# Performance work log

Hardware: AMD Instinct MI355X
Metric: run time of the kernel (lower is better)

Reference implementation:

```python
import jax, jax.numpy as jnp
import numpy as np

B, L, E, H, D, DFF = 2, 2048, 1024, 16, 64, 4096
SCALE = D ** 0.5


def rmsnorm(x):
    # NOTE: original uses mean(x*x)**0.5 with no eps and no learned scale
    rms = jnp.sqrt(jnp.mean(x * x, axis=-1, keepdims=True))
    return x / rms


def alibi_matrix():
    i = jnp.arange(L)
    dists = -jnp.abs(i[None, :] - i[:, None]).astype(jnp.float32)  # [L, L]
    slopes = 2.0 ** (-jnp.linspace(1.0, 8.0, H))                   # [H]
    alibi = slopes[:, None, None] * dists                          # [H, L, L]
    causal = jnp.tril(jnp.ones((L, L), dtype=bool))
    return jnp.where(causal[None], alibi, -jnp.inf)[None]          # [1, H, L, L]


def setup_inputs() -> dict:
    key = jax.random.key(0)
    ks = jax.random.split(key, 16)
    s = 0.02
    return {
        "X": jax.random.normal(ks[0], (B, L, E), jnp.float32),
        "encoder_out": jax.random.normal(ks[1], (B, L, E), jnp.float32),
        # self-attention params
        "Wqkv": jax.random.normal(ks[2], (E, 3 * H * D), jnp.float32) * s,
        "bqkv": jnp.zeros((3 * H * D,), jnp.float32),
        "Wo_sa": jax.random.normal(ks[3], (H * D, E), jnp.float32) * s,
        "bo_sa": jnp.zeros((E,), jnp.float32),
        # cross-attention params (computed by torch module but its forward returns X, so unused)
        "Wq": jax.random.normal(ks[4], (E, H * D), jnp.float32) * s,
        "bq": jnp.zeros((H * D,), jnp.float32),
        "Wkv": jax.random.normal(ks[5], (E, 2 * H * D), jnp.float32) * s,
        "bkv": jnp.zeros((2 * H * D,), jnp.float32),
        "Wo_ca": jax.random.normal(ks[6], (H * D, E), jnp.float32) * s,
        "bo_ca": jnp.zeros((E,), jnp.float32),
        # GLU FFN params (bias=False)
        "Ww": jax.random.normal(ks[7], (E, DFF), jnp.float32) * s,
        "Wv": jax.random.normal(ks[8], (E, DFF), jnp.float32) * s,
        "Wout": jax.random.normal(ks[9], (DFF, E), jnp.float32) * s,
    }


def reference(X, encoder_out, Wqkv, bqkv, Wo_sa, bo_sa, Wq, bq, Wkv, bkv,
              Wo_ca, bo_ca, Ww, Wv, Wout):
    alibi = alibi_matrix()

    # ---- self-attention (pre-norm + residual) ----
    h = rmsnorm(X)
    qkv = (h @ Wqkv + bqkv).reshape(B, L, H, 3, D)
    Q, K, V = qkv[..., 0, :], qkv[..., 1, :], qkv[..., 2, :]      # [B, L, H, D]
    scores = jnp.einsum('blhd,bmhd->bhlm', Q, K) / SCALE + alibi  # [B, H, L, L]
    attn = jax.nn.softmax(scores, axis=-1)
    ctx = jnp.einsum('bhlm,bmhd->blhd', attn, V).reshape(B, L, H * D)
    X = X + ctx @ Wo_sa + bo_sa

    # ---- cross-attention stage ----
    # Faithful to source: CrossAttention.forward returns its input X (the
    # normalized tensor) rather than the attention output, so this block is
    # X + rmsnorm(X). Cross-attn params never affect the output.
    X = X + rmsnorm(X)

    # ---- GLU FFN (pre-norm + residual), exact (erf) GELU as in torch F.gelu ----
    h = rmsnorm(X)
    ff = jax.nn.gelu(h @ Ww, approximate=False) * (h @ Wv)
    X = X + ff @ Wout
    return X
```

## Files before the change

kernel.cpp:

```cpp
#include <hip/hip_runtime.h>

#define B_SZ 2
#define L_SEQ 2048
#define E_DIM 1024
#define NH 16
#define DH 64
#define DFF_DIM 4096
#define ROWS (B_SZ * L_SEQ)
#define NCID 80

typedef __attribute__((ext_vector_type(8))) short short8;
typedef __attribute__((ext_vector_type(4))) float f32x4;

__device__ __forceinline__ short f2bf(float f) {
  unsigned u = __builtin_bit_cast(unsigned, f);
  u = (u + 0x7FFFu + ((u >> 16) & 1u)) >> 16;
  return (short)u;
}
__device__ __forceinline__ float bf2f(short s) {
  unsigned u = ((unsigned)(unsigned short)s) << 16;
  return __builtin_bit_cast(float, u);
}

__device__ __forceinline__ float fast_gelu(float x) {
  float ax = fabsf(x) * 0.70710678118654752f;
  float t = __builtin_amdgcn_rcpf(__builtin_fmaf(0.3275911f, ax, 1.0f));
  float p = t * __builtin_fmaf(
                    t,
                    __builtin_fmaf(
                        t,
                        __builtin_fmaf(t,
                                       __builtin_fmaf(t, 1.061405429f,
                                                      -1.453152027f),
                                       1.421413741f),
                        -0.284496736f),
                    0.254829592f);
  float erf = 1.0f - p * __expf(-ax * ax);
  erf = copysignf(erf, x);
  return 0.5f * x * (1.0f + erf);
}

__device__ __forceinline__ void async_copy16(const void* g, void* l) {
  __builtin_amdgcn_global_load_lds(
      (const __attribute__((address_space(1))) void*)g,
      (__attribute__((address_space(3))) void*)l, 16, 0, 0);
}

__device__ __forceinline__ float block_sum256(float v) {
  __shared__ float sbuf[4];
#pragma unroll
  for (int off = 32; off > 0; off >>= 1) v += __shfl_xor(v, off, 64);
  int lane = threadIdx.x & 63, w = threadIdx.x >> 6;
  if (lane == 0) sbuf[w] = v;
  __syncthreads();
  return sbuf[0] + sbuf[1] + sbuf[2] + sbuf[3];
}

__global__ __launch_bounds__(256) void prep_all(
    const float* __restrict__ Wqkv, const float* __restrict__ Wo,
    const float* __restrict__ Ww, const float* __restrict__ Wv,
    const float* __restrict__ Wout, const float* __restrict__ X,
    short* __restrict__ Bqkv3, short* __restrict__ WoT,
    short* __restrict__ Bcat, short* __restrict__ WoutT,
    short* __restrict__ H) {
  __shared__ float tile[32][33];
  int b = blockIdx.x;
  if (b < 16384) {
    const float* W;
    short* Wt;
    int K, N, mode, bx, by;
    if (b < 3072) {
      W = Wqkv; Wt = Bqkv3; K = 1024; N = 3072; mode = 1;
      bx = b % 96; by = b / 96;
    } else if (b < 4096) {
      int c = b - 3072;
      W = Wo; Wt = WoT; K = 1024; N = 1024; mode = 1;
      bx = c & 31; by = c >> 5;
    } else if (b < 8192) {
      int c = b - 4096;
      W = Ww; Wt = Bcat; K = 1024; N = 4096; mode = 2;
      bx = c & 127; by = c >> 7;
    } else if (b < 12288) {
      int c = b - 8192;
      W = Wv; Wt = Bcat; K = 1024; N = 4096; mode = 3;
      bx = c & 127; by = c >> 7;
    } else {
      int c = b - 12288;
      W = Wout; Wt = WoutT; K = 4096; N = 1024; mode = 1;
      bx = c & 31; by = c >> 5;
    }
    int n0 = bx * 32, k0 = by * 32;
    int tx = threadIdx.x & 31, ty = threadIdx.x >> 5;
#pragma unroll
    for (int i = 0; i < 4; i++)
      tile[ty + 8 * i][tx] = W[(size_t)(k0 + ty + 8 * i) * N + n0 + tx];
    __syncthreads();
#pragma unroll
    for (int i = 0; i < 4; i++) {
      int n = n0 + ty + 8 * i;
      int orow = (mode == 1)
                     ? n
                     : ((n >> 5) * 64 + (n & 31) + (mode == 3 ? 32 : 0));
      Wt[(size_t)orow * K + k0 + tx] = f2bf(tile[tx][ty + 8 * i]);
    }
  } else {
    size_t row = b - 16384;
    float4 v = ((const float4*)(X + row * E_DIM))[threadIdx.x];
    float ss = v.x * v.x + v.y * v.y + v.z * v.z + v.w * v.w;
    ss = block_sum256(ss);
    float inv = rsqrtf(ss * (1.0f / E_DIM));
    short* h = H + row * E_DIM + (size_t)threadIdx.x * 4;
    h[0] = f2bf(v.x * inv);
    h[1] = f2bf(v.y * inv);
    h[2] = f2bf(v.z * inv);
    h[3] = f2bf(v.w * inv);
  }
}

__global__ __launch_bounds__(256) void resid_rms_fused(
    const float* __restrict__ X, const float* __restrict__ P0,
    const float* __restrict__ P1, const float* __restrict__ bias,
    float* __restrict__ Xout, short* __restrict__ H) {
  size_t row = blockIdx.x;
  int t = threadIdx.x;
  float4 v = ((const float4*)(X + row * E_DIM))[t];
  float4 a = ((const float4*)(P0 + row * E_DIM))[t];
  float4 b = ((const float4*)(P1 + row * E_DIM))[t];
  float4 c = ((const float4*)bias)[t];
  v.x += a.x + b.x + c.x;
  v.y += a.y + b.y + c.y;
  v.z += a.z + b.z + c.z;
  v.w += a.w + b.w + c.w;
  float ss = v.x * v.x + v.y * v.y + v.z * v.z + v.w * v.w;
  ss = block_sum256(ss);
  float inv = rsqrtf(ss * (1.0f / E_DIM));
  float4 o;
  o.x = v.x * (1.0f + inv);
  o.y = v.y * (1.0f + inv);
  o.z = v.z * (1.0f + inv);
  o.w = v.w * (1.0f + inv);
  ((float4*)(Xout + row * E_DIM))[t] = o;
  short* h = H + row * E_DIM + (size_t)t * 4;
  h[0] = f2bf(v.x * inv);
  h[1] = f2bf(v.y * inv);
  h[2] = f2bf(v.z * inv);
  h[3] = f2bf(v.w * inv);
}

__global__ __launch_bounds__(256) void add2_k(const float* __restrict__ P0,
                                              const float* __restrict__ P1,
                                              float* __restrict__ out) {
  size_t i = (size_t)blockIdx.x * 256 + threadIdx.x;
  float4 v = ((const float4*)out)[i];
  float4 a = ((const float4*)P0)[i];
  float4 b = ((const float4*)P1)[i];
  v.x += a.x + b.x;
  v.y += a.y + b.y;
  v.z += a.z + b.z;
  v.w += a.w + b.w;
  ((float4*)out)[i] = v;
}

__global__ __launch_bounds__(256, 2) void gemm_bt(
    const short* __restrict__ A, const short* __restrict__ Bt,
    const float* __restrict__ bias, void* __restrict__ out,
    void* __restrict__ out2, void* __restrict__ out3, int M, int N, int K,
    int epi, int ksplit) {
  __shared__ short smem[128 * 32 * 4];
  short* As0 = smem;
  short* Bs0 = smem + 4096;
  short* As1 = smem + 8192;
  short* Bs1 = smem + 12288;
  int t = threadIdx.x;
  int lane = t & 63;
  int quad = lane >> 4, l16 = lane & 15;
  int wave = t >> 6;
  int wr = wave >> 1, wc = wave & 1;
  int m0 = blockIdx.y * 128, n0 = blockIdx.x * 128;
  int klen = K / ksplit;
  int kstart = blockIdx.z * klen;

  f32x4 acc[4][4];
#pragma unroll
  for (int i = 0; i < 4; i++)
#pragma unroll
    for (int j = 0; j < 4; j++) acc[i][j] = (f32x4){0.f, 0.f, 0.f, 0.f};

  for (int k0 = kstart; k0 < kstart + klen; k0 += 64) {
    __syncthreads();
#pragma unroll
    for (int p = 0; p < 2; p++) {
      int s = p * 256 + t;
      int mm = s >> 2, kk = (s & 3) * 8;
      const short* ag = A + (size_t)(m0 + mm) * K + k0 + kk;
      const short* bg = Bt + (size_t)(n0 + mm) * K + k0 + kk;
      async_copy16(ag, As0 + (size_t)s * 8);
      async_copy16(bg, Bs0 + (size_t)s * 8);
      async_copy16(ag + 32, As1 + (size_t)s * 8);
      async_copy16(bg + 32, Bs1 + (size_t)s * 8);
    }
    __syncthreads();
#pragma unroll
    for (int half = 0; half < 2; half++) {
      const short* As = half ? As1 : As0;
      const short* Bs = half ? Bs1 : Bs0;
      short8 af[4], bfv[4];
#pragma unroll
      for (int i = 0; i < 4; i++) {
        af[i] = *(const short8*)&As[(wr * 64 + i * 16 + l16) * 32 + quad * 8];
        bfv[i] = *(const short8*)&Bs[(wc * 64 + i * 16 + l16) * 32 + quad * 8];
      }
#pragma unroll
      for (int mi = 0; mi < 4; mi++)
#pragma unroll
        for (int ni = 0; ni < 4; ni++)
          acc[mi][ni] = __builtin_amdgcn_mfma_f32_16x16x32_bf16(
              af[mi], bfv[ni], acc[mi][ni], 0, 0, 0);
    }
  }

  if (epi == 5) {
    short* FF = (short*)out;
    int ffbase = blockIdx.x * 64 + wc * 32;
#pragma unroll
    for (int mi = 0; mi < 4; mi++)
#pragma unroll
      for (int ni = 0; ni < 2; ni++)
#pragma unroll
        for (int r = 0; r < 4; r++) {
          int rowl = wr * 64 + mi * 16 + quad * 4 + r;
          float g = fast_gelu(acc[mi][ni][r]);
          FF[(size_t)(m0 + rowl) * DFF_DIM + ffbase + ni * 16 + l16] =
              f2bf(g * acc[mi][ni + 2][r]);
        }
    return;
  }

#pragma unroll
  for (int mi = 0; mi < 4; mi++) {
#pragma unroll
    for (int ni = 0; ni < 4; ni++) {
      int col = n0 + wc * 64 + ni * 16 + l16;
#pragma unroll
      for (int r = 0; r < 4; r++) {
        int row = m0 + wr * 64 + mi * 16 + quad * 4 + r;
        float v = acc[mi][ni][r];
        if (epi == 4) {
          float* po = (float*)out + (size_t)blockIdx.z * ((size_t)M * N);
          po[(size_t)row * N + col] = v;
        } else {
          v += bias[col];
          int h = col / 192;
          int rem = col - h * 192;
          int ty = rem >> 6, d = rem & 63;
          short* dst = (ty == 0) ? (short*)out
                                 : ((ty == 1) ? (short*)out2 : (short*)out3);
          int bb = row >> 11, l = row & 2047;
          dst[((size_t)(bb * NH + h) * L_SEQ + l) * DH + d] = f2bf(v);
        }
      }
    }
  }
}

__global__ __launch_bounds__(512, 2) void gemm256(
    const short* __restrict__ A, const short* __restrict__ Bt,
    const float* __restrict__ bias, void* __restrict__ out,
    void* __restrict__ out2, void* __restrict__ out3, int M, int N, int K,
    int epi) {
  __shared__ __align__(16) short smem[65536];
  (void)M;
  (void)N;
  int t = threadIdx.x;
  int lane = t & 63;
  int quad = lane >> 4, l16 = lane & 15;
  int wave = t >> 6;
  int wr = wave >> 2;
  int wc = wave & 3;
  int m0 = blockIdx.y * 256, n0 = blockIdx.x * 256;

  int row0 = t >> 3;
  int sl = (t & 7) ^ (row0 & 7);
  int goff = row0 * K + sl * 8;
  int ldw = t * 16;
  char* smc = (char*)smem;
  auto stageHT = [&](const short* gsrc, int ldsbase) {
    async_copy16(gsrc + goff, smc + ldsbase + ldw);
    async_copy16(gsrc + goff + (K << 6), smc + ldsbase + 8192 + ldw);
  };

  int swz = (l16 & 7) << 4;
  int colp0 = (quad * 16) ^ swz;
  int colp1 = (64 + quad * 16) ^ swz;
  const char* aB = smc + wr * 16384 + l16 * 128;
  const char* bB = smc + 32768 + (wc >> 1) * 16384 + (wc & 1) * 8192 +
                   l16 * 128;

  f32x4 acc[8][4];
#pragma unroll
  for (int i = 0; i < 8; i++)
#pragma unroll
    for (int j = 0; j < 4; j++) acc[i][j] = (f32x4){0.f, 0.f, 0.f, 0.f};
  short8 areg[4][2], breg[4][2];

  const short* Am0 = A + (size_t)m0 * K;
  const short* Am1 = A + (size_t)(m0 + 128) * K;
  const short* Bn0 = Bt + (size_t)n0 * K;
  const short* Bn1 = Bt + (size_t)(n0 + 128) * K;

  stageHT(Am0, 0);
  stageHT(Am1, 16384);
  stageHT(Bn0, 32768);
  stageHT(Bn1, 49152);
  stageHT(Bn0 + 64, 98304);
  stageHT(Bn1 + 64, 114688);
  asm volatile("s_waitcnt vmcnt(4)" ::: "memory");
  __builtin_amdgcn_s_barrier();

  int NJ = K >> 7;
  for (int j = 0; j < NJ; ++j) {
    int kb = j << 7;
    bool lastI = (j == NJ - 1);
#pragma unroll
    for (int ph = 0; ph < 8; ++ph) {
      const int sub = ph & 3;
      const int mq = sub >> 1;
      const int nq = sub & 1;
      const int dOff = (ph >> 2) ? 65536 : 0;
      if (sub == 0 || sub == 2) {
#pragma unroll
        for (int im = 0; im < 4; ++im) {
          areg[im][0] =
              *(const short8*)(aB + dOff + (mq * 4 + im) * 2048 + colp0);
          areg[im][1] =
              *(const short8*)(aB + dOff + (mq * 4 + im) * 2048 + colp1);
        }
      }
      if (sub <= 1) {
#pragma unroll
        for (int in = 0; in < 2; ++in) {
          breg[nq * 2 + in][0] =
              *(const short8*)(bB + dOff + (nq * 2 + in) * 2048 + colp0);
          breg[nq * 2 + in][1] =
              *(const short8*)(bB + dOff + (nq * 2 + in) * 2048 + colp1);
        }
      }
      if (ph == 0) stageHT(Am0 + kb + 64, 65536);
      if (ph == 1) stageHT(Am1 + kb + 64, 65536 + 16384);
      if (!lastI) {
        if (ph == 2) stageHT(Bn0 + kb + 128, 32768);
        if (ph == 3) stageHT(Bn1 + kb + 128, 49152);
        if (ph == 4) stageHT(Am0 + kb + 128, 0);
        if (ph == 5) stageHT(Am1 + kb + 128, 16384);
        if (ph == 6) stageHT(Bn0 + kb + 192, 98304);
        if (ph == 7) stageHT(Bn1 + kb + 192, 114688);
      }
      __builtin_amdgcn_s_barrier();
      asm volatile("s_waitcnt lgkmcnt(0)" ::: "memory");
      __builtin_amdgcn_sched_barrier(0);
      __builtin_amdgcn_s_setprio(1);
#pragma unroll
      for (int im = 0; im < 4; ++im)
#pragma unroll
        for (int in = 0; in < 2; ++in)
#pragma unroll
          for (int kh = 0; kh < 2; ++kh)
            acc[mq * 4 + im][nq * 2 + in] =
                __builtin_amdgcn_mfma_f32_16x16x32_bf16(
                    areg[im][kh], breg[nq * 2 + in][kh],
                    acc[mq * 4 + im][nq * 2 + in], 0, 0, 0);
      __builtin_amdgcn_s_setprio(0);
      if (ph == 3) {
        if (lastI)
          asm volatile("s_waitcnt vmcnt(0)" ::: "memory");
        else
          asm volatile("s_waitcnt vmcnt(4)" ::: "memory");
      }
      if (ph == 7 && !lastI)
        asm volatile("s_waitcnt vmcnt(4)" ::: "memory");
      __builtin_amdgcn_s_barrier();
    }
  }

  if (epi == 5) {
    short* FF = (short*)out;
    int ffbase = (n0 + wc * 64) >> 1;
#pragma unroll
    for (int mi = 0; mi < 8; ++mi)
#pragma unroll
      for (int ni = 0; ni < 2; ++ni)
#pragma unroll
        for (int r = 0; r < 4; ++r) {
          int rowl = wr * 128 + mi * 16 + quad * 4 + r;
          float g = fast_gelu(acc[mi][ni][r]);
          FF[(size_t)(m0 + rowl) * DFF_DIM + ffbase + ni * 16 + l16] =
              f2bf(g * acc[mi][ni + 2][r]);
        }
    return;
  }
#pragma unroll
  for (int mi = 0; mi < 8; ++mi) {
#pragma unroll
    for (int ni = 0; ni < 4; ++ni) {
      int col = n0 + wc * 64 + ni * 16 + l16;
      float bv = bias[col];
      int h = col / 192;
      int rem = col - h * 192;
      int ty = rem >> 6, d = rem & 63;
      short* dst =
          (ty == 0) ? (short*)out : ((ty == 1) ? (short*)out2 : (short*)out3);
#pragma unroll
      for (int r = 0; r < 4; ++r) {
        int row = m0 + wr * 128 + mi * 16 + quad * 4 + r;
        float v = acc[mi][ni][r] + bv;
        int bb = row >> 11, l = row & 2047;
        dst[((size_t)(bb * NH + h) * L_SEQ + l) * DH + d] = f2bf(v);
      }
    }
  }
}

__global__ __launch_bounds__(256) void v_transp(const short* __restrict__ Vh,
                                                short* __restrict__ VTh) {
  int lt = blockIdx.x, bh = blockIdx.y;
  __shared__ short vtile[64 * 72];
  int t = threadIdx.x;
  int r = t >> 3, c = (t & 7) * 8;
  const short* src = Vh + ((size_t)bh * L_SEQ + lt * 64) * DH;
#pragma unroll
  for (int p = 0; p < 2; p++) {
    int row = r + p * 32;
    short8 vv = *(const short8*)(src + (size_t)row * DH + c);
    *(short8*)&vtile[row * 72 + c] = vv;
  }
  __syncthreads();
#pragma unroll
  for (int p = 0; p < 2; p++) {
    int d = r + p * 32;
    short8 o;
#pragma unroll
    for (int u = 0; u < 8; u++) o[u] = vtile[(c + u) * 72 + d];
    *(short8*)(VTh + ((size_t)bh * DH + d) * L_SEQ + lt * 64 + c) = o;
  }
}

__global__ __launch_bounds__(256) void attn_k(const short* __restrict__ Qh,
                                              const short* __restrict__ Kh,
                                              const short* __restrict__ VTh,
                                              float* __restrict__ OP,
                                              float* __restrict__ RS) {
  int cid = blockIdx.x;
  int bh = blockIdx.y;
  int b = bh >> 4, h = bh & 15;
  int qt, ch;
  if (cid < 8) {
    qt = cid; ch = 0;
  } else if (cid < 24) {
    qt = 8 + ((cid - 8) >> 1); ch = (cid - 8) & 1;
  } else if (cid < 48) {
    qt = 16 + (cid - 24) / 3; ch = (cid - 24) % 3;
  } else {
    qt = 24 + ((cid - 48) >> 2); ch = (cid - 48) & 3;
  }
  int t0 = ch * 8;
  int tend = min(t0 + 8, qt + 1);

  int t = threadIdx.x;
  int wave = t >> 6, lane = t & 63;
  int quad = lane >> 4, l16 = lane & 15;

  __shared__ short kt[64 * 72];
  __shared__ short vt[64 * 72];
  __shared__ short pb[4 * 16 * 70];

  const float slope = exp2f(-(1.0f + (7.0f / 15.0f) * (float)h));
  int iw = qt * 64 + wave * 16;

  short8 qf[2];
  {
    const short* qp = Qh + ((size_t)bh * L_SEQ + iw + l16) * DH + quad * 8;
    qf[0] = *(const short8*)(qp);
    qf[1] = *(const short8*)(qp + 32);
  }

  f32x4 o[4];
#pragma unroll
  for (int i = 0; i < 4; i++) o[i] = (f32x4){0.f, 0.f, 0.f, 0.f};
  float rs[4] = {0.f, 0.f, 0.f, 0.f};
  float crow[4];
  int irow[4];
#pragma unroll
  for (int r = 0; r < 4; r++) {
    irow[r] = iw + quad * 4 + r;
    crow[r] = -slope * (float)irow[r] - 8.0f;
  }

  int sr = t >> 3, sc = (t & 7) * 8;
  const short* kg = Kh + (size_t)bh * L_SEQ * DH;
  const short* vg = VTh + (size_t)bh * DH * L_SEQ;
  short8 kreg[2], vreg[2];
  auto loadKV = [&](int j0) {
    kreg[0] = *(const short8*)(kg + (size_t)(j0 + sr) * DH + sc);
    kreg[1] = *(const short8*)(kg + (size_t)(j0 + sr + 32) * DH + sc);
    vreg[0] = *(const short8*)(vg + (size_t)sr * L_SEQ + j0 + sc);
    vreg[1] = *(const short8*)(vg + (size_t)(sr + 32) * L_SEQ + j0 + sc);
  };
  loadKV(t0 * 64);

  short* pw = &pb[wave * 16 * 70];
  for (int tix = t0; tix < tend; ++tix) {
    int j0 = tix * 64;
    __syncthreads();
    *(short8*)&kt[sr * 72 + sc] = kreg[0];
    *(short8*)&kt[(sr + 32) * 72 + sc] = kreg[1];
    *(short8*)&vt[sr * 72 + sc] = vreg[0];
    *(short8*)&vt[(sr + 32) * 72 + sc] = vreg[1];
    __syncthreads();
    if (tix + 1 < tend) loadKV(j0 + 64);

    f32x4 s[4];
#pragma unroll
    for (int nt = 0; nt < 4; nt++) {
      f32x4 a = (f32x4){0.f, 0.f, 0.f, 0.f};
#pragma unroll
      for (int ks = 0; ks < 2; ks++) {
        short8 bf =
            *(const short8*)&kt[(nt * 16 + l16) * 72 + ks * 32 + quad * 8];
        a = __builtin_amdgcn_mfma_f32_16x16x32_bf16(qf[ks], bf, a, 0, 0, 0);
      }
      s[nt] = a;
    }
    bool diag = (tix == qt);
#pragma unroll
    for (int nt = 0; nt < 4; nt++) {
      int j = j0 + nt * 16 + l16;
      float jb = slope * (float)j;
#pragma unroll
      for (int r = 0; r < 4; r++) {
        float v = __builtin_fmaf(s[nt][r], 0.125f, jb + crow[r]);
        if (diag && j > irow[r]) v = -1e30f;
        float p = __expf(v);
        rs[r] += p;
        pw[(quad * 4 + r) * 70 + nt * 16 + l16] = f2bf(p);
      }
    }
    short8 pf[2];
    pf[0] = *(const short8*)&pw[l16 * 70 + quad * 8];
    pf[1] = *(const short8*)&pw[l16 * 70 + 32 + quad * 8];
#pragma unroll
    for (int nt = 0; nt < 4; nt++) {
#pragma unroll
      for (int ks = 0; ks < 2; ks++) {
        short8 bv =
            *(const short8*)&vt[(nt * 16 + l16) * 72 + ks * 32 + quad * 8];
        o[nt] = __builtin_amdgcn_mfma_f32_16x16x32_bf16(pf[ks], bv, o[nt], 0,
                                                        0, 0);
      }
    }
  }
  float* op = OP + ((size_t)bh * NCID + cid) * 64 * 64;
  float* rsp = RS + ((size_t)bh * NCID + cid) * 64;
#pragma unroll
  for (int r = 0; r < 4; r++) {
#pragma unroll
    for (int off = 1; off < 16; off <<= 1) rs[r] += __shfl_xor(rs[r], off, 64);
    int rowl = wave * 16 + quad * 4 + r;
#pragma unroll
    for (int nt = 0; nt < 4; nt++) op[rowl * 64 + nt * 16 + l16] = o[nt][r];
    if (l16 == 0) rsp[rowl] = rs[r];
  }
}

__global__ __launch_bounds__(256) void attn_merge(const float* __restrict__ OP,
                                                  const float* __restrict__ RS,
                                                  short* __restrict__ ctx) {
  int row = blockIdx.x;
  int b = row >> 11, i = row & 2047;
  int qt = i >> 6, rowin = i & 63;
  int base, nch;
  if (qt < 8) {
    base = qt; nch = 1;
  } else if (qt < 16) {
    base = 8 + 2 * (qt - 8); nch = 2;
  } else if (qt < 24) {
    base = 24 + 3 * (qt - 16); nch = 3;
  } else {
    base = 48 + 4 * (qt - 24); nch = 4;
  }
  int t = threadIdx.x;
  int col = t * 4;
  int h = col >> 6;
  int bh = b * NH + h;
  float4 o = {0.f, 0.f, 0.f, 0.f};
  float l = 0.f;
  for (int s = 0; s < nch; s++) {
    size_t cb = ((size_t)bh * NCID + base + s) * 64 + rowin;
    float4 v = *(const float4*)&OP[cb * 64 + (col & 63)];
    o.x += v.x;
    o.y += v.y;
    o.z += v.z;
    o.w += v.w;
    l += RS[cb];
  }
  float inv = 1.0f / l;
  short* dst = ctx + (size_t)row * (NH * DH) + col;
  dst[0] = f2bf(o.x * inv);
  dst[1] = f2bf(o.y * inv);
  dst[2] = f2bf(o.z * inv);
  dst[3] = f2bf(o.w * inv);
}

extern "C" void kernel_launch(void* const* d_in, const int* in_sizes, int n_in,
                              void* d_out, int out_size, void* d_ws,
                              size_t ws_size, hipStream_t stream) {
  const float* X = (const float*)d_in[0];
  const float* Wqkv = (const float*)d_in[2];
  const float* bqkv = (const float*)d_in[3];
  const float* Wo_sa = (const float*)d_in[4];
  const float* bo_sa = (const float*)d_in[5];
  const float* Ww = (const float*)d_in[12];
  const float* Wv = (const float*)d_in[13];
  const float* Wout = (const float*)d_in[14];

  char* ws = (char*)d_ws;
  auto take = [&](size_t bytes) {
    char* p = ws;
    ws += (bytes + 255) & ~(size_t)255;
    return p;
  };
  short* Bqkv3 = (short*)take((size_t)3072 * 1024 * 2);
  short* WoT = (short*)take((size_t)E_DIM * E_DIM * 2);
  short* Bcat = (short*)take((size_t)2 * DFF_DIM * E_DIM * 2);
  short* WoutT = (short*)take((size_t)E_DIM * DFF_DIM * 2);
  short* Hbuf = (short*)take((size_t)ROWS * E_DIM * 2);
  short* Qh = (short*)take((size_t)ROWS * NH * DH * 2);
  short* Kh = (short*)take((size_t)ROWS * NH * DH * 2);
  short* Vh = (short*)take((size_t)ROWS * NH * DH * 2);
  short* VTh = (short*)take((size_t)ROWS * NH * DH * 2);
  short* CTX = (short*)take((size_t)ROWS * NH * DH * 2);
  char* big = take((size_t)48 * 1024 * 1024);
  float* OP = (float*)big;
  float* RS = OP + (size_t)B_SZ * NH * NCID * 64 * 64;
  float* Pwo = (float*)(big + (size_t)16 * 1024 * 1024);
  short* FF = (short*)Pwo;
  float* Pwout = (float*)Qh;
  (void)ws_size;
  (void)in_sizes;
  (void)n_in;
  (void)out_size;

  dim3 blk(256);
  prep_all<<<16384 + ROWS, blk, 0, stream>>>(Wqkv, Wo_sa, Ww, Wv, Wout, X,
                                             Bqkv3, WoT, Bcat, WoutT, Hbuf);
  gemm256<<<dim3(3072 / 256, ROWS / 256), dim3(512), 0, stream>>>(
      Hbuf, Bqkv3, bqkv, Qh, Kh, Vh, ROWS, 3072, 1024, 6);
  v_transp<<<dim3(L_SEQ / 64, B_SZ * NH), blk, 0, stream>>>(Vh, VTh);
  attn_k<<<dim3(NCID, B_SZ * NH), blk, 0, stream>>>(Qh, Kh, VTh, OP, RS);
  attn_merge<<<ROWS, blk, 0, stream>>>(OP, RS, CTX);
  gemm_bt<<<dim3(1024 / 128, ROWS / 128, 2), blk, 0, stream>>>(
      CTX, WoT, nullptr, Pwo, nullptr, nullptr, ROWS, 1024, 1024, 4, 2);
  resid_rms_fused<<<ROWS, blk, 0, stream>>>(
      X, Pwo, Pwo + (size_t)ROWS * E_DIM, bo_sa, (float*)d_out, Hbuf);
  gemm256<<<dim3(2 * DFF_DIM / 256, ROWS / 256), dim3(512), 0, stream>>>(
      Hbuf, Bcat, nullptr, FF, nullptr, nullptr, ROWS, 2 * DFF_DIM, 1024, 5);
  gemm_bt<<<dim3(1024 / 128, ROWS / 128, 2), blk, 0, stream>>>(
      FF, WoutT, nullptr, Pwout, nullptr, nullptr, ROWS, 1024, 4096, 4, 2);
  add2_k<<<ROWS * E_DIM / (256 * 4), blk, 0, stream>>>(
      Pwout, Pwout + (size_t)ROWS * E_DIM, (float*)d_out);
}
```

Before: 413.0 us.

## Swizzle GEMM workgroups across XCDs and double attention KV stage width

Adds an XCD-aware remap of block indices in both GEMM kernels so adjacent output tiles land on the same chiplet and share L2. The attention kernel now stages two 64-key tiles (128 keys) of K and V into LDS per sync pair instead of one. This halves the barrier count and gives more time to overlap the register prefetch. The cost is more LDS and registers per block, which may lower occupancy, and any odd tile count leaves a half-used stage.

```diff
diff --git a/kernel.cpp b/kernel.cpp
--- a/kernel.cpp
+++ b/kernel.cpp
@@ -44,6 +44,17 @@
   __builtin_amdgcn_global_load_lds(
       (const __attribute__((address_space(1))) void*)g,
       (__attribute__((address_space(3))) void*)l, 16, 0, 0);
+}
+
+__device__ __forceinline__ void xcd_swz(int& bx, int& by) {
+  int gx = gridDim.x, gy = gridDim.y;
+  int nwg = gx * gy;
+  if ((nwg & 7) == 0) {
+    int lin = by * gx + bx;
+    int swz = (lin & 7) * (nwg >> 3) + (lin >> 3);
+    by = swz % gy;
+    bx = swz / gy;
+  }
 }
 
 __device__ __forceinline__ float block_sum256(float v) {
@@ -176,7 +187,9 @@
   int quad = lane >> 4, l16 = lane & 15;
   int wave = t >> 6;
   int wr = wave >> 1, wc = wave & 1;
-  int m0 = blockIdx.y * 128, n0 = blockIdx.x * 128;
+  int bx = blockIdx.x, by = blockIdx.y;
+  xcd_swz(bx, by);
+  int m0 = by * 128, n0 = bx * 128;
   int klen = K / ksplit;
   int kstart = blockIdx.z * klen;
 
@@ -221,7 +234,7 @@
 
   if (epi == 5) {
     short* FF = (short*)out;
-    int ffbase = blockIdx.x * 64 + wc * 32;
+    int ffbase = bx * 64 + wc * 32;
 #pragma unroll
     for (int mi = 0; mi < 4; mi++)
 #pragma unroll
@@ -277,7 +290,9 @@
   int wave = t >> 6;
   int wr = wave >> 2;
   int wc = wave & 3;
-  int m0 = blockIdx.y * 256, n0 = blockIdx.x * 256;
+  int bx = blockIdx.x, by = blockIdx.y;
+  xcd_swz(bx, by);
+  int m0 = by * 256, n0 = bx * 256;
 
   int row0 = t >> 3;
   int sl = (t & 7) ^ (row0 & 7);
@@ -469,8 +484,8 @@
   int wave = t >> 6, lane = t & 63;
   int quad = lane >> 4, l16 = lane & 15;
 
-  __shared__ short kt[64 * 72];
-  __shared__ short vt[64 * 72];
+  __shared__ short kt[128 * 72];
+  __shared__ short vt[64 * 136];
   __shared__ short pb[4 * 16 * 70];
 
   const float slope = exp2f(-(1.0f + (7.0f / 15.0f) * (float)h));
@@ -498,63 +513,74 @@
   int sr = t >> 3, sc = (t & 7) * 8;
   const short* kg = Kh + (size_t)bh * L_SEQ * DH;
   const short* vg = VTh + (size_t)bh * DH * L_SEQ;
-  short8 kreg[2], vreg[2];
+  short8 kreg[4], vreg[4];
   auto loadKV = [&](int j0) {
     kreg[0] = *(const short8*)(kg + (size_t)(j0 + sr) * DH + sc);
     kreg[1] = *(const short8*)(kg + (size_t)(j0 + sr + 32) * DH + sc);
+    kreg[2] = *(const short8*)(kg + (size_t)(j0 + sr + 64) * DH + sc);
+    kreg[3] = *(const short8*)(kg + (size_t)(j0 + sr + 96) * DH + sc);
     vreg[0] = *(const short8*)(vg + (size_t)sr * L_SEQ + j0 + sc);
     vreg[1] = *(const short8*)(vg + (size_t)(sr + 32) * L_SEQ + j0 + sc);
+    vreg[2] = *(const short8*)(vg + (size_t)sr * L_SEQ + j0 + 64 + sc);
+    vreg[3] = *(const short8*)(vg + (size_t)(sr + 32) * L_SEQ + j0 + 64 + sc);
   };
   loadKV(t0 * 64);
 
   short* pw = &pb[wave * 16 * 70];
-  for (int tix = t0; tix < tend; ++tix) {
-    int j0 = tix * 64;
+  for (int tp = t0; tp < tend; tp += 2) {
     __syncthreads();
     *(short8*)&kt[sr * 72 + sc] = kreg[0];
     *(short8*)&kt[(sr + 32) * 72 + sc] = kreg[1];
-    *(short8*)&vt[sr * 72 + sc] = vreg[0];
-    *(short8*)&vt[(sr + 32) * 72 + sc] = vreg[1];
+    *(short8*)&kt[(sr + 64) * 72 + sc] = kreg[2];
+    *(short8*)&kt[(sr + 96) * 72 + sc] = kreg[3];
+    *(short8*)&vt[sr * 136 + sc] = vreg[0];
+    *(short8*)&vt[(sr + 32) * 136 + sc] = vreg[1];
+    *(short8*)&vt[sr * 136 + 64 + sc] = vreg[2];
+    *(short8*)&vt[(sr + 32) * 136 + 64 + sc] = vreg[3];
     __syncthreads();
-    if (tix + 1 < tend) loadKV(j0 + 64);
-
-    f32x4 s[4];
-#pragma unroll
-    for (int nt = 0; nt < 4; nt++) {
-      f32x4 a = (f32x4){0.f, 0.f, 0.f, 0.f};
-#pragma unroll
-      for (int ks = 0; ks < 2; ks++) {
-        short8 bf =
-            *(const short8*)&kt[(nt * 16 + l16) * 72 + ks * 32 + quad * 8];
-        a = __builtin_amdgcn_mfma_f32_16x16x32_bf16(qf[ks], bf, a, 0, 0, 0);
-      }
-      s[nt] = a;
-    }
-    bool diag = (tix == qt);
-#pragma unroll
-    for (int nt = 0; nt < 4; nt++) {
-      int j = j0 + nt * 16 + l16;
-      float jb = slope * (float)j;
-#pragma unroll
-      for (int r = 0; r < 4; r++) {
-        float v = __builtin_fmaf(s[nt][r], 0.125f, jb + crow[r]);
-        if (diag && j > irow[r]) v = -1e30f;
-        float p = __expf(v);
-        rs[r] += p;
-        pw[(quad * 4 + r) * 70 + nt * 16 + l16] = f2bf(p);
-      }
-    }
-    short8 pf[2];
-    pf[0] = *(const short8*)&pw[l16 * 70 + quad * 8];
-    pf[1] = *(const short8*)&pw[l16 * 70 + 32 + quad * 8];
-#pragma unroll
-    for (int nt = 0; nt < 4; nt++) {
-#pragma unroll
-      for (int ks = 0; ks < 2; ks++) {
-        short8 bv =
-            *(const short8*)&vt[(nt * 16 + l16) * 72 + ks * 32 + quad * 8];
-        o[nt] = __builtin_amdgcn_mfma_f32_16x16x32_bf16(pf[ks], bv, o[nt], 0,
-                                                        0, 0);
+    if (tp + 2 < tend) loadKV((tp + 2) * 64);
+    int te = min(tp + 2, tend);
+    for (int tix = tp; tix < te; ++tix) {
+      int sub = tix - tp;
+      int j0 = tix * 64;
+      f32x4 s[4];
+#pragma unroll
+      for (int nt = 0; nt < 4; nt++) {
+        f32x4 a = (f32x4){0.f, 0.f, 0.f, 0.f};
+#pragma unroll
+        for (int ks = 0; ks < 2; ks++) {
+          short8 bf = *(const short8*)&kt[(sub * 64 + nt * 16 + l16) * 72 +
+                                          ks * 32 + quad * 8];
+          a = __builtin_amdgcn_mfma_f32_16x16x32_bf16(qf[ks], bf, a, 0, 0, 0);
+        }
+        s[nt] = a;
+      }
+      bool diag = (tix == qt);
+#pragma unroll
+      for (int nt = 0; nt < 4; nt++) {
+        int j = j0 + nt * 16 + l16;
+        float jb = slope * (float)j;
+#pragma unroll
+        for (int r = 0; r < 4; r++) {
+          float v = __builtin_fmaf(s[nt][r], 0.125f, jb + crow[r]);
+          if (diag && j > irow[r]) v = -1e30f;
+          float p = __expf(v);
+          rs[r] += p;
+          pw[(quad * 4 + r) * 70 + nt * 16 + l16] = f2bf(p);
+        }
+      }
+      short8 pf[2];
+      pf[0] = *(const short8*)&pw[l16 * 70 + quad * 8];
+      pf[1] = *(const short8*)&pw[l16 * 70 + 32 + quad * 8];
+#pragma unroll
+      for (int nt = 0; nt < 4; nt++) {
+#pragma unroll
+        for (int ks = 0; ks < 2; ks++) {
+          short8 bv = *(const short8*)&vt[(nt * 16 + l16) * 136 + sub * 64 +
+                                          ks * 32 + quad * 8];
+          o[nt] = __builtin_amdgcn_mfma_f32_16x16x32_bf16(pf[ks], bv, o[nt],
+                                                          0, 0, 0);
+        }
       }
     }
   }
```

After: 415.9 us. Within noise of the previous version (+0.7%).
